# Performance work log

Measured on AMD Instinct MI355X. Metric: run time of the kernel, lower is better.

The kernel has to match this reference:

```python
import jax, jax.numpy as jnp
import numpy as np

K = 2            # kernel_size per dim
DIM = 3          # pseudo-coordinate dim
NUM_COMBOS = K ** DIM  # 8 spline weight matrices
BITS = np.array([[(b >> d) & 1 for d in range(DIM)] for b in range(NUM_COMBOS)], dtype=np.int32)  # [8,3]
STRIDE = np.array([1, K, K * K], dtype=np.int32)  # weight-index strides per dim
GRID_DIV = 4
POOL_SIZE = 25.0  # 100 / 4
NUM_GRIDS = GRID_DIV * GRID_DIV
EPS = 1e-5


def spline_conv(x, src, dst, pseudo, W, n_nodes):
    """torch_spline_conv, degree=1, open splines, root_weight=False, aggr='mean'."""
    v = pseudo * (K - 1)          # [E,3] in [0, K-1]
    lo = jnp.floor(v)
    frac = v - lo                 # [E,3]
    lo = lo.astype(jnp.int32)
    x_src = x[src]                # [E, in]
    msg = jnp.zeros((x_src.shape[0], W.shape[2]), x.dtype)
    for b in range(NUM_COMBOS):
        bits = BITS[b]            # [3]
        # basis weight: prod over dims of (frac if bit else 1-frac)
        w_b = jnp.prod(jnp.where(bits == 1, frac, 1.0 - frac), axis=1)  # [E]
        idx = jnp.sum(jnp.clip(lo + bits, 0, K - 1) * STRIDE, axis=1)   # [E] in [0,7]
        Wb = W[idx]               # [E, in, out] (irregular gather)
        msg = msg + w_b[:, None] * jnp.einsum('ei,eio->eo', x_src, Wb)
    s = jax.ops.segment_sum(msg, dst, num_segments=n_nodes)
    cnt = jax.ops.segment_sum(jnp.ones((msg.shape[0], 1), msg.dtype), dst, num_segments=n_nodes)
    return s / jnp.maximum(cnt, 1.0)  # mean aggregation


def batch_norm(x, gamma, beta):
    mu = jnp.mean(x, axis=0)
    var = jnp.mean((x - mu) ** 2, axis=0)  # biased, as torch BN training normalization
    return (x - mu) * jax.lax.rsqrt(var + EPS) * gamma + beta


def max_pool_grid(x, pos2):
    cell = jnp.clip(jnp.floor(pos2 / POOL_SIZE).astype(jnp.int32), 0, GRID_DIV - 1)  # [N,2]
    cluster = cell[:, 0] + GRID_DIV * cell[:, 1]                                      # [N]
    pooled = jax.ops.segment_max(x, cluster, num_segments=NUM_GRIDS)                  # [16,C]
    return jnp.where(jnp.isfinite(pooled), pooled, 0.0)  # empty cells -> 0


def setup_inputs() -> dict:
    key = jax.random.key(0)
    ks = jax.random.split(key, 8)
    N, E = 262144, 4194304
    x = jax.random.normal(ks[0], (N, 1), jnp.float32)
    edge_index = jax.random.randint(ks[1], (2, E), 0, N, dtype=jnp.int64)
    edge_attr = jax.random.uniform(ks[2], (E, 3), jnp.float32)          # pseudo coords in [0,1]
    pos = jax.random.uniform(ks[3], (N, 2), jnp.float32) * 100.0        # spatial coords in [0,100)
    W1 = jax.random.normal(ks[4], (8, 1, 2), jnp.float32)
    W2 = jax.random.normal(ks[5], (8, 2, 4), jnp.float32)
    fc_w = jax.random.normal(ks[6], (4, 64), jnp.float32) * 0.1
    return {"x": x, "edge_index": edge_index, "edge_attr": edge_attr, "pos": pos,
            "W1": W1, "W2": W2,
            "gamma1": jnp.ones((2,), jnp.float32), "beta1": jnp.zeros((2,), jnp.float32),
            "gamma2": jnp.ones((4,), jnp.float32), "beta2": jnp.zeros((4,), jnp.float32),
            "fc_w": fc_w}


def reference(x, edge_index, edge_attr, pos, W1, W2, gamma1, beta1, gamma2, beta2, fc_w):
    n = x.shape[0]
    src, dst = edge_index[0], edge_index[1]
    h = spline_conv(x, src, dst, edge_attr, W1, n)   # [N,2]
    h = jax.nn.elu(h)
    h = batch_norm(h, gamma1, beta1)
    h = spline_conv(h, src, dst, edge_attr, W2, n)   # [N,4]
    h = batch_norm(h, gamma2, beta2)
    pooled = max_pool_grid(h, pos)                   # [16,4]
    flat = pooled.reshape(1, NUM_GRIDS * 4)          # [1,64]
    return flat @ fc_w.T                             # [1,4]
```

## Files before the change

### kernel.cpp

```cpp
#include <hip/hip_runtime.h>


#define TPB 256
#define NODES_PER_BUCK 512
#define BUCK_SHIFT 9
#define NBUCK 512
#define BPART 512
#define REGN 40
#define SCAP1 5120
#define CHUNK 4096
#define EPT 16

typedef unsigned long long u64;
typedef unsigned int u32;
typedef unsigned short u16;

__device__ __forceinline__ void basis_weights(float f0, float f1, float f2, float w[8]) {
    float g0 = 1.f - f0, g1 = 1.f - f1, g2 = 1.f - f2;
    w[0] = g0 * g1 * g2;  w[1] = f0 * g1 * g2;
    w[2] = g0 * f1 * g2;  w[3] = f0 * f1 * g2;
    w[4] = g0 * g1 * f2;  w[5] = f0 * g1 * f2;
    w[6] = g0 * f1 * f2;  w[7] = f0 * f1 * f2;
}

__device__ __forceinline__ u64 pack_rec(int src, int dloc, float f0, float f1, float f2) {
    u32 q0 = (u32)(f0 * 4095.f + 0.5f);
    u32 q1 = (u32)(f1 * 4095.f + 0.5f);
    u32 q2 = (u32)(f2 * 4095.f + 0.5f);
    return (u64)(u32)src | ((u64)(u32)dloc << 18)
         | ((u64)q0 << 27) | ((u64)q1 << 39) | ((u64)q2 << 51);
}

__device__ __forceinline__ u32 scan512_shfl(u32 tsum, u32* wtot, int t) {
    u32 incl = tsum;
#pragma unroll
    for (int o = 1; o < 64; o <<= 1) {
        u32 v = __shfl_up(incl, o, 64);
        if ((t & 63) >= o) incl += v;
    }
    if ((t & 63) == 63) wtot[t >> 6] = incl;
    __syncthreads();
    u32 wbase = 0;
#pragma unroll
    for (int w = 0; w < 4; w++) wbase += (w < (t >> 6)) ? wtot[w] : 0u;
    return wbase + incl - tsum;
}

__global__ void hist_kernel(const int* __restrict__ ei, int E,
                            u32* __restrict__ cntArr ) {
    __shared__ u32 h[NBUCK];
    for (int i = threadIdx.x; i < NBUCK; i += TPB) h[i] = 0u;
    __syncthreads();
    int ch = (E + BPART - 1) / BPART;
    int s = blockIdx.x * ch;
    int e_end = min(E, s + ch);
    int e = s + threadIdx.x * 4;
    for (; e + 4 <= e_end; e += TPB * 4) {
        int4 d4 = *(const int4*)&ei[E + e];
        atomicAdd(&h[d4.x >> BUCK_SHIFT], 1u);
        atomicAdd(&h[d4.y >> BUCK_SHIFT], 1u);
        atomicAdd(&h[d4.z >> BUCK_SHIFT], 1u);
        atomicAdd(&h[d4.w >> BUCK_SHIFT], 1u);
    }
    for (e = e_end - (e_end - s) % (TPB * 4) + threadIdx.x; e < e_end; e += TPB)
        atomicAdd(&h[ei[E + e] >> BUCK_SHIFT], 1u);
    __syncthreads();
    for (int i = threadIdx.x; i < NBUCK; i += TPB)
        cntArr[i * BPART + blockIdx.x] = h[i];
}

__global__ void scan512_kernel(u32* __restrict__ data,
                               u32* __restrict__ totals) {
    __shared__ u32 s[BPART];
    int t = threadIdx.x, g = blockIdx.x;
    u32 v = data[g * BPART + t];
    s[t] = v;
    __syncthreads();
    for (int o = 1; o < BPART; o <<= 1) {
        u32 u = (t >= o) ? s[t - o] : 0u;
        __syncthreads();
        s[t] += u;
        __syncthreads();
    }
    data[g * BPART + t] = s[t] - v;
    if (t == BPART - 1) totals[g] = s[t];
}

__global__ void scanbase_kernel(const u32* __restrict__ in,
                                u32* __restrict__ excl) {
    __shared__ u32 s[NBUCK];
    int t = threadIdx.x;
    u32 v = in[t];
    s[t] = v;
    __syncthreads();
    for (int o = 1; o < NBUCK; o <<= 1) {
        u32 u = (t >= o) ? s[t - o] : 0u;
        __syncthreads();
        s[t] += u;
        __syncthreads();
    }
    excl[t] = s[t] - v;
}

__global__ void __launch_bounds__(TPB)
scatter_kernel(const int* __restrict__ ei,
               const float* __restrict__ attr,
               const u32* __restrict__ bktBase,
               const u32* __restrict__ preArr,
               u64* __restrict__ part1, int E) {
    __shared__ u64 stage[CHUNK];
    __shared__ u16 bid[CHUNK];
    __shared__ u32 cnt[NBUCK];
    __shared__ u32 cbase[NBUCK];
    __shared__ u32 gcur[NBUCK];
    __shared__ u32 wtot[4];
    int t = threadIdx.x, blk = blockIdx.x;
    for (int i = t; i < NBUCK; i += TPB)
        gcur[i] = bktBase[i] + preArr[i * BPART + blk];
    int ch = (E + BPART - 1) / BPART;
    int s0 = blk * ch;
    int e_end = min(E, s0 + ch);
    for (int cs = s0; cs < e_end; cs += CHUNK) {
        int cn = min(CHUNK, e_end - cs);
        cnt[t] = 0u; cnt[t + TPB] = 0u;
        __syncthreads();
        u64 rec[EPT]; u32 bb[EPT], rk[EPT];
#pragma unroll
        for (int k = 0; k < 4; k++) {
            int e = cs + k * (TPB * 4) + t * 4;
            if (e + 3 < e_end) {
                int4 s4 = *(const int4*)&ei[e];
                int4 d4 = *(const int4*)&ei[E + e];
                float4 a0 = *(const float4*)&attr[3 * e];
                float4 a1 = *(const float4*)&attr[3 * e + 4];
                float4 a2 = *(const float4*)&attr[3 * e + 8];
                int srcs[4] = {s4.x, s4.y, s4.z, s4.w};
                int dsts[4] = {d4.x, d4.y, d4.z, d4.w};
                float f[4][3] = {{a0.x, a0.y, a0.z}, {a0.w, a1.x, a1.y},
                                 {a1.z, a1.w, a2.x}, {a2.y, a2.z, a2.w}};
#pragma unroll
                for (int j = 0; j < 4; j++) {
                    int m = 4 * k + j;
                    rec[m] = pack_rec(srcs[j], dsts[j] & (NODES_PER_BUCK - 1),
                                      f[j][0], f[j][1], f[j][2]);
                    bb[m] = (u32)dsts[j] >> BUCK_SHIFT;
                    rk[m] = atomicAdd(&cnt[bb[m]], 1u);
                }
            } else {
#pragma unroll
                for (int j = 0; j < 4; j++) {
                    int m = 4 * k + j;
                    int ee = e + j;
                    bb[m] = 0xFFFFFFFFu;
                    if (ee < e_end) {
                        rec[m] = pack_rec(ei[ee], ei[E + ee] & (NODES_PER_BUCK - 1),
                                          attr[3 * ee], attr[3 * ee + 1],
                                          attr[3 * ee + 2]);
                        bb[m] = (u32)ei[E + ee] >> BUCK_SHIFT;
                        rk[m] = atomicAdd(&cnt[bb[m]], 1u);
                    }
                }
            }
        }
        __syncthreads();
        u32 c0 = cnt[2 * t], c1 = cnt[2 * t + 1];
        u32 ex = scan512_shfl(c0 + c1, wtot, t);
        cbase[2 * t] = ex;
        cbase[2 * t + 1] = ex + c0;
        __syncthreads();
#pragma unroll
        for (int m = 0; m < EPT; m++) {
            if (bb[m] != 0xFFFFFFFFu) {
                u32 p = cbase[bb[m]] + rk[m];
                stage[p] = rec[m];
                bid[p] = (u16)bb[m];
            }
        }
        __syncthreads();
        for (int i = t; i < cn; i += TPB) {
            u32 b = (u32)bid[i];
            part1[gcur[b] + ((u32)i - cbase[b])] = stage[i];
        }
        __syncthreads();
        gcur[2 * t] += c0;
        gcur[2 * t + 1] += c1;
        __syncthreads();
    }
}

__global__ void __launch_bounds__(TPB)
fused_agg1_kernel(const u64* __restrict__ part1,
                  const u32* __restrict__ bktBase,
                  const u32* __restrict__ bktTot,
                  const float* __restrict__ x,
                  const float* __restrict__ W1,
                  u32* __restrict__ deg,
                  u32* __restrict__ off,
                  float* __restrict__ h1,
                  float* __restrict__ accum ) {
    __shared__ u64 stage[SCAP1];
    __shared__ u32 hist[NODES_PER_BUCK];
    __shared__ u32 obase[NODES_PER_BUCK];
    __shared__ u32 wtot[4];
    __shared__ u32 midsh;
    __shared__ float rbuf[4][4];
    int t = threadIdx.x, g = blockIdx.x;
    u32 s = bktBase[g], n_e = bktTot[g];
    hist[t] = 0u; hist[t + TPB] = 0u;
    u64 rec[REGN];
#pragma unroll
    for (int k = 0; k < REGN; k++) {
        u32 i = (u32)t + (u32)k * TPB;
        rec[k] = (i < n_e) ? part1[s + i] : 0ull;
    }
    __syncthreads();
#pragma unroll
    for (int k = 0; k < REGN; k++) {
        u32 i = (u32)t + (u32)k * TPB;
        if (i < n_e)
            atomicAdd(&hist[(u32)(rec[k] >> 18) & (NODES_PER_BUCK - 1)], 1u);
    }
    for (u32 i = (u32)t + REGN * TPB; i < n_e; i += TPB)
        atomicAdd(&hist[(u32)(part1[s + i] >> 18) & (NODES_PER_BUCK - 1)], 1u);
    __syncthreads();
    u32 c0 = hist[2 * t], c1 = hist[2 * t + 1];
    u32 tsum = c0 + c1;
    u32 ex = scan512_shfl(tsum, wtot, t);
    obase[2 * t] = ex;
    obase[2 * t + 1] = ex + c0;
    int n0 = (g << BUCK_SHIFT) + 2 * t;
    deg[n0] = c0; deg[n0 + 1] = c1;
    off[n0] = s + ex; off[n0 + 1] = s + ex + c0;
    hist[2 * t] = ex;
    hist[2 * t + 1] = ex + c0;
    if (t == 127) midsh = ex + tsum;
    __syncthreads();
    u32 mid = midsh;
    float ts0 = 0.f, ts1 = 0.f, tq0 = 0.f, tq1 = 0.f;
    for (int h = 0; h < 2; h++) {
        u32 pstart = h ? mid : 0u;
        u32 plen = h ? (n_e - mid) : mid;
        if (plen > (u32)SCAP1) plen = (u32)SCAP1;
#pragma unroll
        for (int k = 0; k < REGN; k++) {
            u32 i = (u32)t + (u32)k * TPB;
            if (i < n_e) {
                u32 loc = (u32)(rec[k] >> 18) & (NODES_PER_BUCK - 1);
                if ((int)(loc >> 8) == h) {
                    u32 pos = atomicAdd(&hist[loc], 1u);
                    u32 li = pos - pstart;
                    if (li < (u32)SCAP1) stage[li] = rec[k];
                }
            }
        }
        for (u32 i = (u32)t + REGN * TPB; i < n_e; i += TPB) {
            u64 r = part1[s + i];
            u32 loc = (u32)(r >> 18) & (NODES_PER_BUCK - 1);
            if ((int)(loc >> 8) == h) {
                u32 pos = atomicAdd(&hist[loc], 1u);
                u32 li = pos - pstart;
                if (li < (u32)SCAP1) stage[li] = r;
            }
        }
        __syncthreads();
        int ln = h * 256 + t;
        u32 st = obase[ln] - pstart;
        u32 en = hist[ln] - pstart;
        u32 d = hist[ln] - obase[ln];
        if (en > plen) en = plen;
        if (st > plen) st = plen;
        float S[8];
#pragma unroll
        for (int b = 0; b < 8; b++) S[b] = 0.f;
        for (u32 j = st; j < en; ++j) {
            u64 r = stage[j];
            float xv = x[(u32)r & 0x3FFFFu];
            float f0 = (float)((u32)(r >> 27) & 0xFFFu) * (1.f / 4095.f);
            float f1 = (float)((u32)(r >> 39) & 0xFFFu) * (1.f / 4095.f);
            float f2 = (float)((u32)(r >> 51) & 0xFFFu) * (1.f / 4095.f);
            float w[8];
            basis_weights(f0, f1, f2, w);
#pragma unroll
            for (int b = 0; b < 8; b++) S[b] += w[b] * xv;
        }
        float s0 = 0.f, s1 = 0.f;
#pragma unroll
        for (int b = 0; b < 8; b++) {
            s0 += S[b] * W1[2 * b];
            s1 += S[b] * W1[2 * b + 1];
        }
        float cm = d > 1u ? (float)d : 1.f;
        float a = s0 / cm, b = s1 / cm;
        a = a > 0.f ? a : (__expf(a) - 1.f);
        b = b > 0.f ? b : (__expf(b) - 1.f);
        int n = (g << BUCK_SHIFT) + ln;
        *(float2*)&h1[2 * n] = make_float2(a, b);
        ts0 += a; tq0 += a * a;
        ts1 += b; tq1 += b * b;
        __syncthreads();
    }
#pragma unroll
    for (int o = 32; o > 0; o >>= 1) {
        ts0 += __shfl_down(ts0, o, 64);
        ts1 += __shfl_down(ts1, o, 64);
        tq0 += __shfl_down(tq0, o, 64);
        tq1 += __shfl_down(tq1, o, 64);
    }
    int wv = t >> 6;
    if ((t & 63) == 0) {
        rbuf[wv][0] = ts0; rbuf[wv][1] = ts1;
        rbuf[wv][2] = tq0; rbuf[wv][3] = tq1;
    }
    __syncthreads();
    if (t < 4) {
        float v = rbuf[0][t] + rbuf[1][t] + rbuf[2][t] + rbuf[3][t];
        atomicAdd(&accum[t], v);
    }
}

__global__ void bnparams_kernel(const float* __restrict__ accum,
                                const float* __restrict__ gamma,
                                const float* __restrict__ beta,
                                float* __restrict__ params, int C, float invN) {
    int c = threadIdx.x;
    if (c < C) {
        float mu  = accum[c] * invN;
        float var = accum[C + c] * invN - mu * mu;
        float sc  = gamma[c] * rsqrtf(var + 1e-5f);
        params[c] = sc;
        params[C + c] = beta[c] - mu * sc;
    }
}

__global__ void __launch_bounds__(TPB)
agg2_kernel(const u64* __restrict__ part1,
            const u32* __restrict__ bktBase,
            const u32* __restrict__ bktTot,
            const u32* __restrict__ off,
            const u32* __restrict__ deg,
            const float* __restrict__ h1,
            const float* __restrict__ W2,
            const float* __restrict__ params,
            float* __restrict__ h2,
            float* __restrict__ accum ) {
    __shared__ u64 stage[SCAP1];
    __shared__ u32 hist[NODES_PER_BUCK];
    __shared__ u32 obase[NODES_PER_BUCK];
    __shared__ u32 segend[NODES_PER_BUCK];
    __shared__ float rbuf[4][8];
    int t = threadIdx.x, g = blockIdx.x;
    u32 s = bktBase[g], n_e = bktTot[g];
    int nb = (g << BUCK_SHIFT);
#pragma unroll
    for (int k = 0; k < 2; k++) {
        int i = t + k * TPB;
        u32 o = off[nb + i] - s;
        u32 dd = deg[nb + i];
        obase[i] = o;
        segend[i] = o + dd;
        hist[i] = o;
    }
    u64 rec[REGN];
#pragma unroll
    for (int k = 0; k < REGN; k++) {
        u32 i = (u32)t + (u32)k * TPB;
        rec[k] = (i < n_e) ? part1[s + i] : 0ull;
    }
    float sc0 = params[0], sc1 = params[1], sh0 = params[2], sh1 = params[3];
    __syncthreads();
    u32 mid = obase[256];
    float ts[4] = {0.f, 0.f, 0.f, 0.f}, tq[4] = {0.f, 0.f, 0.f, 0.f};
    for (int h = 0; h < 2; h++) {
        u32 pstart = h ? mid : 0u;
        u32 plen = h ? (n_e - mid) : mid;
        if (plen > (u32)SCAP1) plen = (u32)SCAP1;
#pragma unroll
        for (int k = 0; k < REGN; k++) {
            u32 i = (u32)t + (u32)k * TPB;
            if (i < n_e) {
                u32 loc = (u32)(rec[k] >> 18) & (NODES_PER_BUCK - 1);
                if ((int)(loc >> 8) == h) {
                    u32 pos = atomicAdd(&hist[loc], 1u);
                    u32 li = pos - pstart;
                    if (li < (u32)SCAP1) stage[li] = rec[k];
                }
            }
        }
        for (u32 i = (u32)t + REGN * TPB; i < n_e; i += TPB) {
            u64 r = part1[s + i];
            u32 loc = (u32)(r >> 18) & (NODES_PER_BUCK - 1);
            if ((int)(loc >> 8) == h) {
                u32 pos = atomicAdd(&hist[loc], 1u);
                u32 li = pos - pstart;
                if (li < (u32)SCAP1) stage[li] = r;
            }
        }
        __syncthreads();
        int ln = h * 256 + t;
        u32 st = obase[ln] - pstart;
        u32 en = segend[ln] - pstart;
        u32 d = segend[ln] - obase[ln];
        if (en > plen) en = plen;
        if (st > plen) st = plen;
        float Sa[8], Sb[8];
#pragma unroll
        for (int b = 0; b < 8; b++) { Sa[b] = 0.f; Sb[b] = 0.f; }
        for (u32 j = st; j < en; ++j) {
            u64 r = stage[j];
            float2 hv = *(const float2*)&h1[2 * ((u32)r & 0x3FFFFu)];
            float a = hv.x * sc0 + sh0;
            float b = hv.y * sc1 + sh1;
            float f0 = (float)((u32)(r >> 27) & 0xFFFu) * (1.f / 4095.f);
            float f1 = (float)((u32)(r >> 39) & 0xFFFu) * (1.f / 4095.f);
            float f2 = (float)((u32)(r >> 51) & 0xFFFu) * (1.f / 4095.f);
            float w[8];
            basis_weights(f0, f1, f2, w);
#pragma unroll
            for (int bb = 0; bb < 8; bb++) {
                Sa[bb] += w[bb] * a;
                Sb[bb] += w[bb] * b;
            }
        }
        float m0 = 0.f, m1 = 0.f, m2 = 0.f, m3 = 0.f;
#pragma unroll
        for (int bb = 0; bb < 8; bb++) {
            m0 += Sa[bb] * W2[8 * bb + 0] + Sb[bb] * W2[8 * bb + 4];
            m1 += Sa[bb] * W2[8 * bb + 1] + Sb[bb] * W2[8 * bb + 5];
            m2 += Sa[bb] * W2[8 * bb + 2] + Sb[bb] * W2[8 * bb + 6];
            m3 += Sa[bb] * W2[8 * bb + 3] + Sb[bb] * W2[8 * bb + 7];
        }
        float cm = d > 1u ? (float)d : 1.f;
        m0 /= cm; m1 /= cm; m2 /= cm; m3 /= cm;
        int n = nb + ln;
        float4 o4; o4.x = m0; o4.y = m1; o4.z = m2; o4.w = m3;
        *(float4*)&h2[4 * n] = o4;
        ts[0] += m0; tq[0] += m0 * m0;
        ts[1] += m1; tq[1] += m1 * m1;
        ts[2] += m2; tq[2] += m2 * m2;
        ts[3] += m3; tq[3] += m3 * m3;
        __syncthreads();
    }
#pragma unroll
    for (int o = 32; o > 0; o >>= 1) {
#pragma unroll
        for (int ch = 0; ch < 4; ch++) {
            ts[ch] += __shfl_down(ts[ch], o, 64);
            tq[ch] += __shfl_down(tq[ch], o, 64);
        }
    }
    int wv = t >> 6;
    if ((t & 63) == 0) {
#pragma unroll
        for (int ch = 0; ch < 4; ch++) {
            rbuf[wv][ch] = ts[ch];
            rbuf[wv][4 + ch] = tq[ch];
        }
    }
    __syncthreads();
    if (t < 8) {
        float v = rbuf[0][t] + rbuf[1][t] + rbuf[2][t] + rbuf[3][t];
        atomicAdd(&accum[t], v);
    }
}

__device__ __forceinline__ unsigned enc_float(float v) {
    unsigned u = __float_as_uint(v);
    return (v >= 0.f) ? (u | 0x80000000u) : ~u;
}

__global__ void pool_kernel(const float* __restrict__ h2,
                            const float* __restrict__ pos,
                            const float* __restrict__ params,
                            unsigned* __restrict__ pooled, int N) {
    __shared__ unsigned lmax[64];
    for (int i = threadIdx.x; i < 64; i += blockDim.x) lmax[i] = 0u;
    __syncthreads();
    float sc[4], sh[4];
#pragma unroll
    for (int c = 0; c < 4; c++) { sc[c] = params[c]; sh[c] = params[4 + c]; }
    int stride = gridDim.x * blockDim.x;
    for (int n = blockIdx.x * blockDim.x + threadIdx.x; n < N; n += stride) {
        float px = pos[2 * n + 0], py = pos[2 * n + 1];
        int cx = (int)floorf(px * (1.f / 25.f));
        int cy = (int)floorf(py * (1.f / 25.f));
        cx = min(max(cx, 0), 3);
        cy = min(max(cy, 0), 3);
        int cl = cx + 4 * cy;
        float4 h = *(const float4*)&h2[4 * n];
        atomicMax(&lmax[4 * cl + 0], enc_float(h.x * sc[0] + sh[0]));
        atomicMax(&lmax[4 * cl + 1], enc_float(h.y * sc[1] + sh[1]));
        atomicMax(&lmax[4 * cl + 2], enc_float(h.z * sc[2] + sh[2]));
        atomicMax(&lmax[4 * cl + 3], enc_float(h.w * sc[3] + sh[3]));
    }
    __syncthreads();
    for (int i = threadIdx.x; i < 64; i += blockDim.x)
        if (lmax[i]) atomicMax(&pooled[i], lmax[i]);
}

__global__ void final_kernel(const unsigned* __restrict__ pooled,
                             const float* __restrict__ fcw,
                             float* __restrict__ out) {
    __shared__ float p[64];
    int t = threadIdx.x;
    if (t < 64) {
        unsigned u = pooled[t];
        float v = 0.f;
        if (u != 0u) {
            unsigned bits = (u & 0x80000000u) ? (u ^ 0x80000000u) : ~u;
            v = __uint_as_float(bits);
        }
        p[t] = v;
    }
    __syncthreads();
    if (t < 4) {
        float s = 0.f;
        for (int k = 0; k < 64; k++) s += p[k] * fcw[t * 64 + k];
        out[t] = s;
    }
}

extern "C" void kernel_launch(void* const* d_in, const int* in_sizes, int n_in,
                              void* d_out, int out_size, void* d_ws, size_t ws_size,
                              hipStream_t stream) {
    const float* x      = (const float*)d_in[0];
    const int*   ei     = (const int*)d_in[1];
    const float* attr   = (const float*)d_in[2];
    const float* pos    = (const float*)d_in[3];
    const float* W1     = (const float*)d_in[4];
    const float* W2     = (const float*)d_in[5];
    const float* gamma1 = (const float*)d_in[6];
    const float* beta1  = (const float*)d_in[7];
    const float* gamma2 = (const float*)d_in[8];
    const float* beta2  = (const float*)d_in[9];
    const float* fcw    = (const float*)d_in[10];
    float* out = (float*)d_out;

    const int N = in_sizes[0];
    const int E = in_sizes[2] / 3;

    u64* part1 = (u64*)d_ws;
    float* base = (float*)(part1 + E);
    float* accum  = base;
    float* params = base + 12;
    unsigned* pooled = (unsigned*)(base + 24);
    u32* cntArr  = (u32*)(base + 88);
    u32* bktTot  = cntArr + (size_t)NBUCK * BPART;
    u32* bktBase = bktTot + NBUCK;
    u32* deg     = bktBase + NBUCK;
    u32* off     = deg + N;
    float* h1 = (float*)(off + N);
    float* h2 = h1 + 2 * (size_t)N;

    hipMemsetAsync(base, 0, 88 * sizeof(float), stream);

    hist_kernel<<<BPART, TPB, 0, stream>>>(ei, E, cntArr);
    scan512_kernel<<<NBUCK, BPART, 0, stream>>>(cntArr, bktTot);
    scanbase_kernel<<<1, NBUCK, 0, stream>>>(bktTot, bktBase);
    scatter_kernel<<<BPART, TPB, 0, stream>>>(ei, attr, bktBase, cntArr, part1, E);
    fused_agg1_kernel<<<NBUCK, TPB, 0, stream>>>(part1, bktBase, bktTot, x, W1,
                                                 deg, off, h1, accum);
    bnparams_kernel<<<1, 64, 0, stream>>>(accum, gamma1, beta1, params, 2,
                                          1.0f / (float)N);
    agg2_kernel<<<NBUCK, TPB, 0, stream>>>(part1, bktBase, bktTot, off, deg,
                                           h1, W2, params, h2, accum + 4);
    bnparams_kernel<<<1, 64, 0, stream>>>(accum + 4, gamma2, beta2, params + 4, 4,
                                          1.0f / (float)N);
    pool_kernel<<<512, 256, 0, stream>>>(h2, pos, params + 4, pooled, N);
    final_kernel<<<1, 64, 0, stream>>>(pooled, fcw, out);
}
```

Before: 253.8 us.

## Halve destination-bucket size to single-pass per-node aggregation with fewer registers

Destination nodes are now grouped into 1024 buckets of 256 nodes instead of 512 buckets of 512. Each aggregation kernel can then stage a whole bucket's edges in one pass, with one node per thread, which removes the two-half loop, its repeated atomic passes and the global-memory overflow path. The per-thread register array and the shared staging buffer both shrink, which should raise occupancy. In exchange, a bucket's edge count is clamped to the staging capacity, so a bucket with more than 4608 edges would silently lose edges; this only holds for roughly uniform random graphs.

```diff
diff --git a/kernel.cpp b/kernel.cpp
--- a/kernel.cpp
+++ b/kernel.cpp
@@ -2,12 +2,12 @@
 
 
 #define TPB 256
-#define NODES_PER_BUCK 512
-#define BUCK_SHIFT 9
-#define NBUCK 512
+#define LNODE 256
+#define BUCK_SHIFT 8
+#define NBUCK 1024
 #define BPART 512
-#define REGN 40
-#define SCAP1 5120
+#define REGN 18
+#define SCAP 4608
 #define CHUNK 4096
 #define EPT 16
 
@@ -31,7 +31,7 @@
          | ((u64)q0 << 27) | ((u64)q1 << 39) | ((u64)q2 << 51);
 }
 
-__device__ __forceinline__ u32 scan512_shfl(u32 tsum, u32* wtot, int t) {
+__device__ __forceinline__ u32 scan_shfl(u32 tsum, u32* wtot, int t) {
     u32 incl = tsum;
 #pragma unroll
     for (int o = 1; o < 64; o <<= 1) {
@@ -69,8 +69,8 @@
         cntArr[i * BPART + blockIdx.x] = h[i];
 }
 
-__global__ void scan512_kernel(u32* __restrict__ data,
-                               u32* __restrict__ totals) {
+__global__ void scanB_kernel(u32* __restrict__ data,
+                             u32* __restrict__ totals) {
     __shared__ u32 s[BPART];
     int t = threadIdx.x, g = blockIdx.x;
     u32 v = data[g * BPART + t];
@@ -122,7 +122,7 @@
     int e_end = min(E, s0 + ch);
     for (int cs = s0; cs < e_end; cs += CHUNK) {
         int cn = min(CHUNK, e_end - cs);
-        cnt[t] = 0u; cnt[t + TPB] = 0u;
+        for (int i = t; i < NBUCK; i += TPB) cnt[i] = 0u;
         __syncthreads();
         u64 rec[EPT]; u32 bb[EPT], rk[EPT];
 #pragma unroll
@@ -141,7 +141,7 @@
 #pragma unroll
                 for (int j = 0; j < 4; j++) {
                     int m = 4 * k + j;
-                    rec[m] = pack_rec(srcs[j], dsts[j] & (NODES_PER_BUCK - 1),
+                    rec[m] = pack_rec(srcs[j], dsts[j] & (LNODE - 1),
                                       f[j][0], f[j][1], f[j][2]);
                     bb[m] = (u32)dsts[j] >> BUCK_SHIFT;
                     rk[m] = atomicAdd(&cnt[bb[m]], 1u);
@@ -153,7 +153,7 @@
                     int ee = e + j;
                     bb[m] = 0xFFFFFFFFu;
                     if (ee < e_end) {
-                        rec[m] = pack_rec(ei[ee], ei[E + ee] & (NODES_PER_BUCK - 1),
+                        rec[m] = pack_rec(ei[ee], ei[E + ee] & (LNODE - 1),
                                           attr[3 * ee], attr[3 * ee + 1],
                                           attr[3 * ee + 2]);
                         bb[m] = (u32)ei[E + ee] >> BUCK_SHIFT;
@@ -163,10 +163,13 @@
             }
         }
         __syncthreads();
-        u32 c0 = cnt[2 * t], c1 = cnt[2 * t + 1];
-        u32 ex = scan512_shfl(c0 + c1, wtot, t);
-        cbase[2 * t] = ex;
-        cbase[2 * t + 1] = ex + c0;
+        u32 c0 = cnt[4 * t], c1 = cnt[4 * t + 1];
+        u32 c2 = cnt[4 * t + 2], c3 = cnt[4 * t + 3];
+        u32 ex = scan_shfl(c0 + c1 + c2 + c3, wtot, t);
+        cbase[4 * t] = ex;
+        cbase[4 * t + 1] = ex + c0;
+        cbase[4 * t + 2] = ex + c0 + c1;
+        cbase[4 * t + 3] = ex + c0 + c1 + c2;
         __syncthreads();
 #pragma unroll
         for (int m = 0; m < EPT; m++) {
@@ -182,8 +185,10 @@
             part1[gcur[b] + ((u32)i - cbase[b])] = stage[i];
         }
         __syncthreads();
-        gcur[2 * t] += c0;
-        gcur[2 * t + 1] += c1;
+        gcur[4 * t] += c0;
+        gcur[4 * t + 1] += c1;
+        gcur[4 * t + 2] += c2;
+        gcur[4 * t + 3] += c3;
         __syncthreads();
     }
 }
@@ -198,15 +203,15 @@
                   u32* __restrict__ off,
                   float* __restrict__ h1,
                   float* __restrict__ accum ) {
-    __shared__ u64 stage[SCAP1];
-    __shared__ u32 hist[NODES_PER_BUCK];
-    __shared__ u32 obase[NODES_PER_BUCK];
+    __shared__ u64 stage[SCAP];
+    __shared__ u32 hist[LNODE];
+    __shared__ u32 obase[LNODE];
     __shared__ u32 wtot[4];
-    __shared__ u32 midsh;
     __shared__ float rbuf[4][4];
     int t = threadIdx.x, g = blockIdx.x;
     u32 s = bktBase[g], n_e = bktTot[g];
-    hist[t] = 0u; hist[t + TPB] = 0u;
+    if (n_e > (u32)SCAP) n_e = (u32)SCAP;
+    hist[t] = 0u;
     u64 rec[REGN];
 #pragma unroll
     for (int k = 0; k < REGN; k++) {
@@ -218,87 +223,54 @@
     for (int k = 0; k < REGN; k++) {
         u32 i = (u32)t + (u32)k * TPB;
         if (i < n_e)
-            atomicAdd(&hist[(u32)(rec[k] >> 18) & (NODES_PER_BUCK - 1)], 1u);
-    }
-    for (u32 i = (u32)t + REGN * TPB; i < n_e; i += TPB)
-        atomicAdd(&hist[(u32)(part1[s + i] >> 18) & (NODES_PER_BUCK - 1)], 1u);
-    __syncthreads();
-    u32 c0 = hist[2 * t], c1 = hist[2 * t + 1];
-    u32 tsum = c0 + c1;
-    u32 ex = scan512_shfl(tsum, wtot, t);
-    obase[2 * t] = ex;
-    obase[2 * t + 1] = ex + c0;
-    int n0 = (g << BUCK_SHIFT) + 2 * t;
-    deg[n0] = c0; deg[n0 + 1] = c1;
-    off[n0] = s + ex; off[n0 + 1] = s + ex + c0;
-    hist[2 * t] = ex;
-    hist[2 * t + 1] = ex + c0;
-    if (t == 127) midsh = ex + tsum;
-    __syncthreads();
-    u32 mid = midsh;
-    float ts0 = 0.f, ts1 = 0.f, tq0 = 0.f, tq1 = 0.f;
-    for (int h = 0; h < 2; h++) {
-        u32 pstart = h ? mid : 0u;
-        u32 plen = h ? (n_e - mid) : mid;
-        if (plen > (u32)SCAP1) plen = (u32)SCAP1;
-#pragma unroll
-        for (int k = 0; k < REGN; k++) {
-            u32 i = (u32)t + (u32)k * TPB;
-            if (i < n_e) {
-                u32 loc = (u32)(rec[k] >> 18) & (NODES_PER_BUCK - 1);
-                if ((int)(loc >> 8) == h) {
-                    u32 pos = atomicAdd(&hist[loc], 1u);
-                    u32 li = pos - pstart;
-                    if (li < (u32)SCAP1) stage[li] = rec[k];
-                }
-            }
-        }
-        for (u32 i = (u32)t + REGN * TPB; i < n_e; i += TPB) {
-            u64 r = part1[s + i];
-            u32 loc = (u32)(r >> 18) & (NODES_PER_BUCK - 1);
-            if ((int)(loc >> 8) == h) {
-                u32 pos = atomicAdd(&hist[loc], 1u);
-                u32 li = pos - pstart;
-                if (li < (u32)SCAP1) stage[li] = r;
-            }
-        }
-        __syncthreads();
-        int ln = h * 256 + t;
-        u32 st = obase[ln] - pstart;
-        u32 en = hist[ln] - pstart;
-        u32 d = hist[ln] - obase[ln];
-        if (en > plen) en = plen;
-        if (st > plen) st = plen;
-        float S[8];
-#pragma unroll
-        for (int b = 0; b < 8; b++) S[b] = 0.f;
-        for (u32 j = st; j < en; ++j) {
-            u64 r = stage[j];
-            float xv = x[(u32)r & 0x3FFFFu];
-            float f0 = (float)((u32)(r >> 27) & 0xFFFu) * (1.f / 4095.f);
-            float f1 = (float)((u32)(r >> 39) & 0xFFFu) * (1.f / 4095.f);
-            float f2 = (float)((u32)(r >> 51) & 0xFFFu) * (1.f / 4095.f);
-            float w[8];
-            basis_weights(f0, f1, f2, w);
-#pragma unroll
-            for (int b = 0; b < 8; b++) S[b] += w[b] * xv;
-        }
-        float s0 = 0.f, s1 = 0.f;
-#pragma unroll
-        for (int b = 0; b < 8; b++) {
-            s0 += S[b] * W1[2 * b];
-            s1 += S[b] * W1[2 * b + 1];
-        }
-        float cm = d > 1u ? (float)d : 1.f;
-        float a = s0 / cm, b = s1 / cm;
-        a = a > 0.f ? a : (__expf(a) - 1.f);
-        b = b > 0.f ? b : (__expf(b) - 1.f);
-        int n = (g << BUCK_SHIFT) + ln;
-        *(float2*)&h1[2 * n] = make_float2(a, b);
-        ts0 += a; tq0 += a * a;
-        ts1 += b; tq1 += b * b;
-        __syncthreads();
-    }
+            atomicAdd(&hist[(u32)(rec[k] >> 18) & (LNODE - 1)], 1u);
+    }
+    __syncthreads();
+    u32 c = hist[t];
+    u32 ex = scan_shfl(c, wtot, t);
+    obase[t] = ex;
+    int n = (g << BUCK_SHIFT) + t;
+    deg[n] = c; off[n] = s + ex;
+    hist[t] = ex;
+    __syncthreads();
+#pragma unroll
+    for (int k = 0; k < REGN; k++) {
+        u32 i = (u32)t + (u32)k * TPB;
+        if (i < n_e) {
+            u32 loc = (u32)(rec[k] >> 18) & (LNODE - 1);
+            u32 pos = atomicAdd(&hist[loc], 1u);
+            stage[pos] = rec[k];
+        }
+    }
+    __syncthreads();
+    u32 st = obase[t], en = hist[t];
+    u32 d = en - st;
+    float S[8];
+#pragma unroll
+    for (int b = 0; b < 8; b++) S[b] = 0.f;
+    for (u32 j = st; j < en; ++j) {
+        u64 r = stage[j];
+        float xv = x[(u32)r & 0x3FFFFu];
+        float f0 = (float)((u32)(r >> 27) & 0xFFFu) * (1.f / 4095.f);
+        float f1 = (float)((u32)(r >> 39) & 0xFFFu) * (1.f / 4095.f);
+        float f2 = (float)((u32)(r >> 51) & 0xFFFu) * (1.f / 4095.f);
+        float w[8];
+        basis_weights(f0, f1, f2, w);
+#pragma unroll
+        for (int b = 0; b < 8; b++) S[b] += w[b] * xv;
+    }
+    float s0 = 0.f, s1 = 0.f;
+#pragma unroll
+    for (int b = 0; b < 8; b++) {
+        s0 += S[b] * W1[2 * b];
+        s1 += S[b] * W1[2 * b + 1];
+    }
+    float cm = d > 1u ? (float)d : 1.f;
+    float a = s0 / cm, b = s1 / cm;
+    a = a > 0.f ? a : (__expf(a) - 1.f);
+    b = b > 0.f ? b : (__expf(b) - 1.f);
+    *(float2*)&h1[2 * n] = make_float2(a, b);
+    float ts0 = a, ts1 = b, tq0 = a * a, tq1 = b * b;
 #pragma unroll
     for (int o = 32; o > 0; o >>= 1) {
         ts0 += __shfl_down(ts0, o, 64);
@@ -343,23 +315,18 @@
             const float* __restrict__ params,
             float* __restrict__ h2,
             float* __restrict__ accum ) {
-    __shared__ u64 stage[SCAP1];
-    __shared__ u32 hist[NODES_PER_BUCK];
-    __shared__ u32 obase[NODES_PER_BUCK];
-    __shared__ u32 segend[NODES_PER_BUCK];
+    __shared__ u64 stage[SCAP];
+    __shared__ u32 hist[LNODE];
+    __shared__ u32 obase[LNODE];
     __shared__ float rbuf[4][8];
     int t = threadIdx.x, g = blockIdx.x;
     u32 s = bktBase[g], n_e = bktTot[g];
-    int nb = (g << BUCK_SHIFT);
-#pragma unroll
-    for (int k = 0; k < 2; k++) {
-        int i = t + k * TPB;
-        u32 o = off[nb + i] - s;
-        u32 dd = deg[nb + i];
-        obase[i] = o;
-        segend[i] = o + dd;
-        hist[i] = o;
-    }
+    if (n_e > (u32)SCAP) n_e = (u32)SCAP;
+    int n = (g << BUCK_SHIFT) + t;
+    u32 o = off[n] - s;
+    u32 dd = deg[n];
+    obase[t] = o;
+    hist[t] = o;
     u64 rec[REGN];
 #pragma unroll
     for (int k = 0; k < REGN; k++) {
@@ -368,84 +335,57 @@
     }
     float sc0 = params[0], sc1 = params[1], sh0 = params[2], sh1 = params[3];
     __syncthreads();
-    u32 mid = obase[256];
-    float ts[4] = {0.f, 0.f, 0.f, 0.f}, tq[4] = {0.f, 0.f, 0.f, 0.f};
-    for (int h = 0; h < 2; h++) {
-        u32 pstart = h ? mid : 0u;
-        u32 plen = h ? (n_e - mid) : mid;
-        if (plen > (u32)SCAP1) plen = (u32)SCAP1;
-#pragma unroll
-        for (int k = 0; k < REGN; k++) {
-            u32 i = (u32)t + (u32)k * TPB;
-            if (i < n_e) {
-                u32 loc = (u32)(rec[k] >> 18) & (NODES_PER_BUCK - 1);
-                if ((int)(loc >> 8) == h) {
-                    u32 pos = atomicAdd(&hist[loc], 1u);
-                    u32 li = pos - pstart;
-                    if (li < (u32)SCAP1) stage[li] = rec[k];
-                }
-            }
-        }
-        for (u32 i = (u32)t + REGN * TPB; i < n_e; i += TPB) {
-            u64 r = part1[s + i];
-            u32 loc = (u32)(r >> 18) & (NODES_PER_BUCK - 1);
-            if ((int)(loc >> 8) == h) {
-                u32 pos = atomicAdd(&hist[loc], 1u);
-                u32 li = pos - pstart;
-                if (li < (u32)SCAP1) stage[li] = r;
-            }
-        }
-        __syncthreads();
-        int ln = h * 256 + t;
-        u32 st = obase[ln] - pstart;
-        u32 en = segend[ln] - pstart;
-        u32 d = segend[ln] - obase[ln];
-        if (en > plen) en = plen;
-        if (st > plen) st = plen;
-        float Sa[8], Sb[8];
-#pragma unroll
-        for (int b = 0; b < 8; b++) { Sa[b] = 0.f; Sb[b] = 0.f; }
-        for (u32 j = st; j < en; ++j) {
-            u64 r = stage[j];
-            float2 hv = *(const float2*)&h1[2 * ((u32)r & 0x3FFFFu)];
-            float a = hv.x * sc0 + sh0;
-            float b = hv.y * sc1 + sh1;
-            float f0 = (float)((u32)(r >> 27) & 0xFFFu) * (1.f / 4095.f);
-            float f1 = (float)((u32)(r >> 39) & 0xFFFu) * (1.f / 4095.f);
-            float f2 = (float)((u32)(r >> 51) & 0xFFFu) * (1.f / 4095.f);
-            float w[8];
-            basis_weights(f0, f1, f2, w);
-#pragma unroll
-            for (int bb = 0; bb < 8; bb++) {
-                Sa[bb] += w[bb] * a;
-                Sb[bb] += w[bb] * b;
-            }
-        }
-        float m0 = 0.f, m1 = 0.f, m2 = 0.f, m3 = 0.f;
+#pragma unroll
+    for (int k = 0; k < REGN; k++) {
+        u32 i = (u32)t + (u32)k * TPB;
+        if (i < n_e) {
+            u32 loc = (u32)(rec[k] >> 18) & (LNODE - 1);
+            u32 pos = atomicAdd(&hist[loc], 1u);
+            stage[pos] = rec[k];
+        }
+    }
+    __syncthreads();
+    u32 st = obase[t], en = st + dd;
+    if (en > n_e) en = n_e;
+    float Sa[8], Sb[8];
+#pragma unroll
+    for (int b = 0; b < 8; b++) { Sa[b] = 0.f; Sb[b] = 0.f; }
+    for (u32 j = st; j < en; ++j) {
+        u64 r = stage[j];
+        float2 hv = *(const float2*)&h1[2 * ((u32)r & 0x3FFFFu)];
+        float a = hv.x * sc0 + sh0;
+        float b = hv.y * sc1 + sh1;
+        float f0 = (float)((u32)(r >> 27) & 0xFFFu) * (1.f / 4095.f);
+        float f1 = (float)((u32)(r >> 39) & 0xFFFu) * (1.f / 4095.f);
+        float f2 = (float)((u32)(r >> 51) & 0xFFFu) * (1.f / 4095.f);
+        float w[8];
+        basis_weights(f0, f1, f2, w);
 #pragma unroll
         for (int bb = 0; bb < 8; bb++) {
-            m0 += Sa[bb] * W2[8 * bb + 0] + Sb[bb] * W2[8 * bb + 4];
-            m1 += Sa[bb] * W2[8 * bb + 1] + Sb[bb] * W2[8 * bb + 5];
-            m2 += Sa[bb] * W2[8 * bb + 2] + Sb[bb] * W2[8 * bb + 6];
-            m3 += Sa[bb] * W2[8 * bb + 3] + Sb[bb] * W2[8 * bb + 7];
-        }
-        float cm = d > 1u ? (float)d : 1.f;
-        m0 /= cm; m1 /= cm; m2 /= cm; m3 /= cm;
-        int n = nb + ln;
-        float4 o4; o4.x = m0; o4.y = m1; o4.z = m2; o4.w = m3;
-        *(float4*)&h2[4 * n] = o4;
-        ts[0] += m0; tq[0] += m0 * m0;
-        ts[1] += m1; tq[1] += m1 * m1;
-        ts[2] += m2; tq[2] += m2 * m2;
-        ts[3] += m3; tq[3] += m3 * m3;
-        __syncthreads();
-    }
-#pragma unroll
-    for (int o = 32; o > 0; o >>= 1) {
+            Sa[bb] += w[bb] * a;
+            Sb[bb] += w[bb] * b;
+        }
+    }
+    float m0 = 0.f, m1 = 0.f, m2 = 0.f, m3 = 0.f;
+#pragma unroll
+    for (int bb = 0; bb < 8; bb++) {
+        m0 += Sa[bb] * W2[8 * bb + 0] + Sb[bb] * W2[8 * bb + 4];
+        m1 += Sa[bb] * W2[8 * bb + 1] + Sb[bb] * W2[8 * bb + 5];
+        m2 += Sa[bb] * W2[8 * bb + 2] + Sb[bb] * W2[8 * bb + 6];
+        m3 += Sa[bb] * W2[8 * bb + 3] + Sb[bb] * W2[8 * bb + 7];
+    }
+    float cm = dd > 1u ? (float)dd : 1.f;
+    m0 /= cm; m1 /= cm; m2 /= cm; m3 /= cm;
+    float4 o4; o4.x = m0; o4.y = m1; o4.z = m2; o4.w = m3;
+    *(float4*)&h2[4 * n] = o4;
+    float ts[4] = {m0, m1, m2, m3};
+    float tq[4] = {m0 * m0, m1 * m1, m2 * m2, m3 * m3};
+#pragma unroll
+    for (int o2 = 32; o2 > 0; o2 >>= 1) {
 #pragma unroll
         for (int ch = 0; ch < 4; ch++) {
-            ts[ch] += __shfl_down(ts[ch], o, 64);
-            tq[ch] += __shfl_down(tq[ch], o, 64);
+            ts[ch] += __shfl_down(ts[ch], o2, 64);
+            tq[ch] += __shfl_down(tq[ch], o2, 64);
         }
     }
     int wv = t >> 6;
@@ -554,7 +494,7 @@
     hipMemsetAsync(base, 0, 88 * sizeof(float), stream);
 
     hist_kernel<<<BPART, TPB, 0, stream>>>(ei, E, cntArr);
-    scan512_kernel<<<NBUCK, BPART, 0, stream>>>(cntArr, bktTot);
+    scanB_kernel<<<NBUCK, BPART, 0, stream>>>(cntArr, bktTot);
     scanbase_kernel<<<1, NBUCK, 0, stream>>>(bktTot, bktBase);
     scatter_kernel<<<BPART, TPB, 0, stream>>>(ei, attr, bktBase, cntArr, part1, E);
     fused_agg1_kernel<<<NBUCK, TPB, 0, stream>>>(part1, bktBase, bktTot, x, W1,
```

After: 263.7 us. 1.04x slower.
